# Kernel optimization log

Hardware: AMD Instinct MI355X
Metric: run time of the kernel (lower is better)

Reference implementation:

```python
import jax, jax.numpy as jnp
import numpy as np

D = 64   # hidden dim (input_dim == hidden_dims[i] == 64)
L = 6    # GNN layers per NBFNet
EPS = 1e-5

def _layer_norm(x, g, b):
    m = jnp.mean(x, axis=-1, keepdims=True)
    v = jnp.var(x, axis=-1, keepdims=True)
    return (x - m) * jax.lax.rsqrt(v + EPS) * g + b

def _conv(x, boundary, relation, edge_index, edge_type, W, b, g, bt):
    # GeneralizedRelationalConv: distmult message, sum aggregation with
    # boundary self-loop message, linear([input, agg]) -> LayerNorm -> ReLU.
    src, dst = edge_index[0], edge_index[1]
    msg = x[:, src, :] * relation[:, edge_type, :]                # [B,E,D]
    agg = boundary + jnp.zeros_like(x).at[:, dst, :].add(msg)     # edge_weight == 1
    out = jnp.einsum('bnf,fo->bno', jnp.concatenate([x, agg], axis=-1), W) + b
    return jax.nn.relu(_layer_norm(out, g, bt))

def _rel_model(q_rel, rel_edge_index, rel_edge_type, num_rel_nodes,
               rel_emb, Wr, br, gr, btr):
    # RelNBFNet.bellmanford: query = ones, boundary scatter at query relation node.
    B = q_rel.shape[0]
    query = jnp.ones((B, D), dtype=rel_emb.dtype)
    boundary = jnp.zeros((B, num_rel_nodes, D), rel_emb.dtype).at[jnp.arange(B), q_rel].add(query)
    relation = jnp.broadcast_to(rel_emb[None], (B,) + rel_emb.shape)  # dependent=False embedding
    def step(x, p):
        W, b, g, bt = p
        h = _conv(x, boundary, relation, rel_edge_index, rel_edge_type, W, b, g, bt)
        return h + x, None  # short_cut residual
    x, _ = jax.lax.scan(step, boundary, (Wr, br, gr, btr))
    return x  # [B, R, D]  (concat_hidden=False -> hiddens[-1])

def _ent_model(rel_repr, h_index, r_index, t_index, edge_index, edge_type,
               num_nodes, Wp1, bp1, Wp2, bp2, We, be, ge, bte, W1, b1, W2, b2):
    B = h_index.shape[0]
    query = rel_repr[jnp.arange(B), r_index]                      # [B,D]
    boundary = jnp.zeros((B, num_nodes, D), query.dtype).at[jnp.arange(B), h_index].add(query)
    def step(x, p):
        wp1, b1p, wp2, b2p, W, b, g, bt = p
        # project_relations=True: per-layer 2-layer MLP on relation representations
        rel = jax.nn.relu(rel_repr @ wp1 + b1p) @ wp2 + b2p       # [B,R,D]
        h = _conv(x, boundary, rel, edge_index, edge_type, W, b, g, bt)
        return h + x, None
    x, _ = jax.lax.scan(step, boundary, (Wp1, bp1, Wp2, bp2, We, be, ge, bte))
    node_query = jnp.broadcast_to(query[:, None, :], x.shape)
    feat = jnp.concatenate([x, node_query], axis=-1)              # [B,N,2D]
    feat = feat[jnp.arange(B)[:, None], t_index]                  # gather tails [B,K,2D]
    h = jax.nn.relu(feat @ W1 + b1)                               # num_mlp_layers=2
    return (h @ W2 + b2)[..., 0]                                  # [B,K]

def setup_inputs() -> dict:
    key = jax.random.key(0)
    ks = jax.random.split(key, 16)
    B, K, N, E, R, Er = 4, 256, 20000, 200000, 200, 4000
    ND = 100  # direct relations; R = 2*ND
    h = jax.random.randint(ks[0], (B,), 0, N)
    r = jax.random.randint(ks[1], (B,), 0, ND)
    t = jax.random.randint(ks[2], (B, K), 0, N)
    batch = jnp.stack([jnp.broadcast_to(h[:, None], (B, K)), t,
                       jnp.broadcast_to(r[:, None], (B, K))], axis=-1)
    s = 0.05
    return dict(
        batch=batch,
        edge_index=jax.random.randint(ks[3], (2, E), 0, N),
        edge_type=jax.random.randint(ks[4], (E,), 0, R),
        rel_edge_index=jax.random.randint(ks[5], (2, Er), 0, R),
        rel_edge_type=jax.random.randint(ks[6], (Er,), 0, 4),
        num_nodes=N, num_rel_nodes=R,
        rel_emb=jax.random.normal(ks[7], (4, D)) * s,
        Wr=jax.random.normal(ks[8], (L, 2 * D, D)) * s,
        br=jnp.zeros((L, D)), gr=jnp.ones((L, D)), btr=jnp.zeros((L, D)),
        Wp1=jax.random.normal(ks[9], (L, D, D)) * s,
        bp1=jnp.zeros((L, D)),
        Wp2=jax.random.normal(ks[10], (L, D, D)) * s,
        bp2=jnp.zeros((L, D)),
        We=jax.random.normal(ks[11], (L, 2 * D, D)) * s,
        be=jnp.zeros((L, D)), ge=jnp.ones((L, D)), bte=jnp.zeros((L, D)),
        W1=jax.random.normal(ks[12], (2 * D, 2 * D)) * s,
        b1=jnp.zeros((2 * D,)),
        W2=jax.random.normal(ks[13], (2 * D, 1)) * s,
        b2=jnp.zeros((1,)),
    )

def reference(batch, edge_index, edge_type, rel_edge_index, rel_edge_type,
              num_nodes, num_rel_nodes,
              rel_emb, Wr, br, gr, btr,
              Wp1, bp1, Wp2, bp2, We, be, ge, bte, W1, b1, W2, b2):
    # batch holds tail-negative triples (h, t, r) with constant h and r per row,
    # so negative_sample_to_tail is the identity here (eval mode: no edge removal).
    h_index = batch[:, 0, 0]
    t_index = batch[:, :, 1]
    r_index = batch[:, 0, 2]
    rel_repr = _rel_model(r_index, rel_edge_index, rel_edge_type, num_rel_nodes,
                          rel_emb, Wr, br, gr, btr)
    return _ent_model(rel_repr, h_index, r_index, t_index, edge_index, edge_type,
                      num_nodes, Wp1, bp1, Wp2, bp2, We, be, ge, bte, W1, b1, W2, b2)
```

## Files before the change

kernel.cpp:

```cpp
#include <hip/hip_runtime.h>
#include <hip/hip_bf16.h>

#define D_   64
#define L_   6
#define B_   4
#define K_   256
#define NN   20000
#define EE   200000
#define RR   200
#define ER_  4000
#define EPS_ 1e-5f

typedef unsigned short u16;
typedef unsigned int   u32;
typedef short bf16x8 __attribute__((ext_vector_type(8)));
typedef float f32x4  __attribute__((ext_vector_type(4)));

__device__ __forceinline__ u16 f2bf(float f) {
    u32 u = __float_as_uint(f);
    u += 0x7FFF + ((u >> 16) & 1);
    return (u16)(u >> 16);
}
__device__ __forceinline__ u32 pack2bf(float a, float b) {
    return (u32)f2bf(a) | ((u32)f2bf(b) << 16);
}
__device__ __forceinline__ float bflo(u32 u) { return __uint_as_float(u << 16); }
__device__ __forceinline__ float bfhi(u32 u) { return __uint_as_float(u & 0xFFFF0000u); }

__global__ __launch_bounds__(256)
void k_zero2(int* __restrict__ ec, int* __restrict__ rc) {
    int i = blockIdx.x * 256 + threadIdx.x;
    if (i < NN) ec[i] = 0;
    else if (i < NN + RR) rc[i - NN] = 0;
}

__global__ __launch_bounds__(256)
void k_hist2(const int* __restrict__ ei, const int* __restrict__ rei,
             int* __restrict__ ec, int* __restrict__ rc) {
    int g = blockIdx.x * 256 + threadIdx.x;
    if (g < EE) atomicAdd(&ec[ei[EE + g]], 1);
    else if (g < EE + ER_) atomicAdd(&rc[rei[ER_ + (g - EE)]], 1);
}

__global__ __launch_bounds__(256)
void k_scan1_2(const int* __restrict__ e_counts, int* __restrict__ e_pre, int* __restrict__ e_bs,
               const int* __restrict__ r_counts, int* __restrict__ r_pre, int* __restrict__ r_bs,
               int ent_nb) {
    __shared__ int tsum[256];
    const int* counts; int* pre; int* bs; int n; int blk;
    if ((int)blockIdx.x < ent_nb) { counts = e_counts; pre = e_pre; bs = e_bs; n = NN; blk = blockIdx.x; }
    else                          { counts = r_counts; pre = r_pre; bs = r_bs; n = RR; blk = 0; }
    int tid = threadIdx.x;
    int base = blk * 1024 + tid * 4;
    int c0 = 0, c1 = 0, c2 = 0, c3 = 0;
    if (base + 0 < n) c0 = counts[base + 0];
    if (base + 1 < n) c1 = counts[base + 1];
    if (base + 2 < n) c2 = counts[base + 2];
    if (base + 3 < n) c3 = counts[base + 3];
    tsum[tid] = c0 + c1 + c2 + c3;
    __syncthreads();
    if (tid == 0) {
        int acc = 0;
        for (int i = 0; i < 256; i++) { int t = tsum[i]; tsum[i] = acc; acc += t; }
    }
    __syncthreads();
    int run = tsum[tid];
    if (base + 0 < n) pre[base + 0] = run; run += c0;
    if (base + 1 < n) pre[base + 1] = run; run += c1;
    if (base + 2 < n) pre[base + 2] = run; run += c2;
    if (base + 3 < n) pre[base + 3] = run; run += c3;
    if (tid == 255) bs[blk] = run;
}

__global__ __launch_bounds__(64)
void k_scan2_2(int* __restrict__ eb, int enb, int* __restrict__ etot,
               int* __restrict__ rb, int rnb, int* __restrict__ rtot) {
    if (threadIdx.x == 0) {
        int acc = 0;
        for (int i = 0; i < enb; i++) { int t = eb[i]; eb[i] = acc; acc += t; }
        *etot = acc;
    }
    if (threadIdx.x == 1) {
        int acc = 0;
        for (int i = 0; i < rnb; i++) { int t = rb[i]; rb[i] = acc; acc += t; }
        *rtot = acc;
    }
}

__global__ __launch_bounds__(256)
void k_scan3_2(int* __restrict__ e_rp, const int* __restrict__ e_bs, int* __restrict__ e_cur,
               int* __restrict__ r_rp, const int* __restrict__ r_bs, int* __restrict__ r_cur) {
    int i = blockIdx.x * 256 + threadIdx.x;
    if (i < NN) {
        int v = e_rp[i] + e_bs[i >> 10];
        e_rp[i] = v; e_cur[i] = v;
    } else if (i < NN + RR) {
        int j = i - NN;
        int v = r_rp[j] + r_bs[j >> 10];
        r_rp[j] = v; r_cur[j] = v;
    }
}

__global__ __launch_bounds__(256)
void k_fill2(const int* __restrict__ ei, const int* __restrict__ et,
             const int* __restrict__ rei, const int* __restrict__ ret,
             int* __restrict__ e_cur, int* __restrict__ r_cur,
             int* __restrict__ e_packed, int* __restrict__ r_packed) {
    int g = blockIdx.x * 256 + threadIdx.x;
    if (g < EE) {
        int pos = atomicAdd(&e_cur[ei[EE + g]], 1);
        e_packed[pos] = ei[g] | (et[g] << 15);
    } else if (g < EE + ER_) {
        int h = g - EE;
        int pos = atomicAdd(&r_cur[rei[ER_ + h]], 1);
        r_packed[pos] = rei[h] | (ret[h] << 15);
    }
}

template<int NNODES, int MODE, bool FIRST>
__global__ __launch_bounds__(256)
void k_layer9(const float* __restrict__ xin, float* __restrict__ xout,
              const u16* __restrict__ xbin, u16* __restrict__ xbout,
              const void* __restrict__ relv,
              const int* __restrict__ rowptr, const int* __restrict__ packed,
              const float* __restrict__ query, const int* __restrict__ batch,
              const float* __restrict__ W, const float* __restrict__ bias,
              const float* __restrict__ gw, const float* __restrict__ bt) {
    __shared__ u16 Wt[64][72];
    __shared__ u16 As[16][72];
    __shared__ u16 Xs[16][72];
    __shared__ float LNbuf[16][68];
    const int tid   = threadIdx.x;
    const int node0 = blockIdx.x * 4;
    const int lane  = tid & 63;
    const int wv    = tid >> 6;

    int bn0 = batch[0 * K_ * 3 + (MODE ? 0 : 2)];
    int bn1 = batch[1 * K_ * 3 + (MODE ? 0 : 2)];
    int bn2 = batch[2 * K_ * 3 + (MODE ? 0 : 2)];
    int bn3 = batch[3 * K_ * 3 + (MODE ? 0 : 2)];

    const int gnode = node0 + wv;
    int beg = 0, end = 0;
    if (gnode < NNODES) { beg = rowptr[gnode]; end = rowptr[gnode + 1]; }

    const int erow  = wv * 4 + (lane >> 4);
    const int tx    = lane & 15;
    float4 resf = make_float4(0.f, 0.f, 0.f, 0.f);
    if constexpr (!FIRST) {
        int b = erow >> 2, nd = node0 + (erow & 3);
        if (nd < NNODES)
            resf = *reinterpret_cast<const float4*>(
                xin + ((size_t)b * NNODES + nd) * 64 + tx * 4);
    }

    {
        int n = lane, k16 = wv * 16;
        u32 buf[8];
        #pragma unroll
        for (int j2 = 0; j2 < 8; j2++) {
            float w0 = W[(64 + k16 + 2 * j2    ) * 64 + n];
            float w1 = W[(64 + k16 + 2 * j2 + 1) * 64 + n];
            buf[j2] = pack2bf(w0, w1);
        }
        uint4* dst = reinterpret_cast<uint4*>(&Wt[n][k16]);
        dst[0] = make_uint4(buf[0], buf[1], buf[2], buf[3]);
        dst[1] = make_uint4(buf[4], buf[5], buf[6], buf[7]);
    }

    if (tid < 128) {
        int m = tid >> 3, o8 = (tid & 7) * 8;
        int b = m >> 2, node = node0 + (m & 3);
        uint4 v = make_uint4(0, 0, 0, 0);
        if (node < NNODES) {
            if constexpr (FIRST) {
                int bnb = (b==0)?bn0:(b==1)?bn1:(b==2)?bn2:bn3;
                if (node == bnb) {
                    if constexpr (MODE == 1) {
                        const float* q = query + b * 64 + o8;
                        v = make_uint4(pack2bf(q[0], q[1]), pack2bf(q[2], q[3]),
                                       pack2bf(q[4], q[5]), pack2bf(q[6], q[7]));
                    } else {
                        v = make_uint4(0x3F803F80u, 0x3F803F80u, 0x3F803F80u, 0x3F803F80u);
                    }
                }
            } else if constexpr (MODE == 1) {
                v = *reinterpret_cast<const uint4*>(
                    xbin + ((size_t)b * NNODES + node) * 64 + o8);
            } else {
                const float* src = xin + ((size_t)b * NNODES + node) * 64 + o8;
                float4 x0 = *reinterpret_cast<const float4*>(src);
                float4 x1 = *reinterpret_cast<const float4*>(src + 4);
                v = make_uint4(pack2bf(x0.x, x0.y), pack2bf(x0.z, x0.w),
                               pack2bf(x1.x, x1.y), pack2bf(x1.z, x1.w));
            }
        }
        *reinterpret_cast<uint4*>(&Xs[m][o8]) = v;
    }

    const int slot = lane >> 3;
    const int d8   = lane & 7;

    float qreg[4][8];
    if constexpr (MODE == 1) {
        #pragma unroll
        for (int b = 0; b < 4; b++) {
            float4 q0 = *reinterpret_cast<const float4*>(query + b * 64 + d8 * 8);
            float4 q1 = *reinterpret_cast<const float4*>(query + b * 64 + d8 * 8 + 4);
            qreg[b][0]=q0.x; qreg[b][1]=q0.y; qreg[b][2]=q0.z; qreg[b][3]=q0.w;
            qreg[b][4]=q1.x; qreg[b][5]=q1.y; qreg[b][6]=q1.z; qreg[b][7]=q1.w;
        }
    }

    {
        float acc[4][8];
        #pragma unroll
        for (int b = 0; b < 4; b++)
            #pragma unroll
            for (int i = 0; i < 8; i++) acc[b][i] = 0.f;

        for (int e0 = beg; e0 < end; e0 += 16) {
            #pragma unroll
            for (int half = 0; half < 2; half++) {
                int e = e0 + half * 8 + slot;
                if (e < end) {
                    int p = packed[e];
                    int src = p & 0x7FFF;
                    int et  = p >> 15;
                    if constexpr (MODE == 1) {
                        const u16* rb = (const u16*)relv;
                        if constexpr (FIRST) {
                            #pragma unroll
                            for (int b = 0; b < 4; b++) {
                                int bnb = (b==0)?bn0:(b==1)?bn1:(b==2)?bn2:bn3;
                                if (src == bnb) {
                                    uint4 rv = *reinterpret_cast<const uint4*>(
                                        rb + ((size_t)(b * RR + et)) * 64 + d8 * 8);
                                    acc[b][0] = fmaf(qreg[b][0], bflo(rv.x), acc[b][0]);
                                    acc[b][1] = fmaf(qreg[b][1], bfhi(rv.x), acc[b][1]);
                                    acc[b][2] = fmaf(qreg[b][2], bflo(rv.y), acc[b][2]);
                                    acc[b][3] = fmaf(qreg[b][3], bfhi(rv.y), acc[b][3]);
                                    acc[b][4] = fmaf(qreg[b][4], bflo(rv.z), acc[b][4]);
                                    acc[b][5] = fmaf(qreg[b][5], bfhi(rv.z), acc[b][5]);
                                    acc[b][6] = fmaf(qreg[b][6], bflo(rv.w), acc[b][6]);
                                    acc[b][7] = fmaf(qreg[b][7], bfhi(rv.w), acc[b][7]);
                                }
                            }
                        } else {
                            #pragma unroll
                            for (int b = 0; b < 4; b++) {
                                uint4 xv = *reinterpret_cast<const uint4*>(
                                    xbin + ((size_t)(b * NNODES + src)) * 64 + d8 * 8);
                                uint4 rv = *reinterpret_cast<const uint4*>(
                                    ((const u16*)relv) + ((size_t)(b * RR + et)) * 64 + d8 * 8);
                                acc[b][0] = fmaf(bflo(xv.x), bflo(rv.x), acc[b][0]);
                                acc[b][1] = fmaf(bfhi(xv.x), bfhi(rv.x), acc[b][1]);
                                acc[b][2] = fmaf(bflo(xv.y), bflo(rv.y), acc[b][2]);
                                acc[b][3] = fmaf(bfhi(xv.y), bfhi(rv.y), acc[b][3]);
                                acc[b][4] = fmaf(bflo(xv.z), bflo(rv.z), acc[b][4]);
                                acc[b][5] = fmaf(bfhi(xv.z), bfhi(rv.z), acc[b][5]);
                                acc[b][6] = fmaf(bflo(xv.w), bflo(rv.w), acc[b][6]);
                                acc[b][7] = fmaf(bfhi(xv.w), bfhi(rv.w), acc[b][7]);
                            }
                        }
                    } else {
                        const float* re = (const float*)relv;
                        if constexpr (FIRST) {
                            bool m0 = (src == bn0), m1 = (src == bn1),
                                 m2 = (src == bn2), m3 = (src == bn3);
                            if (m0 | m1 | m2 | m3) {
                                float4 r0 = *reinterpret_cast<const float4*>(re + et * 64 + d8 * 8);
                                float4 r1 = *reinterpret_cast<const float4*>(re + et * 64 + d8 * 8 + 4);
                                float rr[8] = {r0.x,r0.y,r0.z,r0.w,r1.x,r1.y,r1.z,r1.w};
                                if (m0) {
                                    #pragma unroll
                                    for (int i = 0; i < 8; i++) acc[0][i] += rr[i];
                                }
                                if (m1) {
                                    #pragma unroll
                                    for (int i = 0; i < 8; i++) acc[1][i] += rr[i];
                                }
                                if (m2) {
                                    #pragma unroll
                                    for (int i = 0; i < 8; i++) acc[2][i] += rr[i];
                                }
                                if (m3) {
                                    #pragma unroll
                                    for (int i = 0; i < 8; i++) acc[3][i] += rr[i];
                                }
                            }
                        } else {
                            float4 r0 = *reinterpret_cast<const float4*>(re + et * 64 + d8 * 8);
                            float4 r1 = *reinterpret_cast<const float4*>(re + et * 64 + d8 * 8 + 4);
                            #pragma unroll
                            for (int b = 0; b < 4; b++) {
                                const float* xr = xin + ((size_t)(b * NNODES + src)) * 64 + d8 * 8;
                                float4 x0 = *reinterpret_cast<const float4*>(xr);
                                float4 x1 = *reinterpret_cast<const float4*>(xr + 4);
                                acc[b][0] = fmaf(x0.x, r0.x, acc[b][0]);
                                acc[b][1] = fmaf(x0.y, r0.y, acc[b][1]);
                                acc[b][2] = fmaf(x0.z, r0.z, acc[b][2]);
                                acc[b][3] = fmaf(x0.w, r0.w, acc[b][3]);
                                acc[b][4] = fmaf(x1.x, r1.x, acc[b][4]);
                                acc[b][5] = fmaf(x1.y, r1.y, acc[b][5]);
                                acc[b][6] = fmaf(x1.z, r1.z, acc[b][6]);
                                acc[b][7] = fmaf(x1.w, r1.w, acc[b][7]);
                            }
                        }
                    }
                }
            }
        }

        #pragma unroll
        for (int b = 0; b < 4; b++)
            #pragma unroll
            for (int i = 0; i < 8; i++) {
                float v = acc[b][i];
                v += __shfl_xor(v, 8);
                v += __shfl_xor(v, 16);
                v += __shfl_xor(v, 32);
                acc[b][i] = v;
            }

        if (slot < 4) {
            float out[8];
            #pragma unroll
            for (int i = 0; i < 8; i++)
                out[i] = (slot==0) ? acc[0][i] : (slot==1) ? acc[1][i]
                       : (slot==2) ? acc[2][i] : acc[3][i];
            int bnb = (slot==0)?bn0:(slot==1)?bn1:(slot==2)?bn2:bn3;
            if (gnode < NNODES && gnode == bnb) {
                if constexpr (MODE == 1) {
                    #pragma unroll
                    for (int i = 0; i < 8; i++)
                        out[i] += (slot==0)?qreg[0][i]:(slot==1)?qreg[1][i]
                                 :(slot==2)?qreg[2][i]:qreg[3][i];
                } else {
                    #pragma unroll
                    for (int i = 0; i < 8; i++) out[i] += 1.0f;
                }
            }
            int m = slot * 4 + wv;
            *reinterpret_cast<uint4*>(&As[m][d8 * 8]) =
                make_uint4(pack2bf(out[0], out[1]), pack2bf(out[2], out[3]),
                           pack2bf(out[4], out[5]), pack2bf(out[6], out[7]));
        }
    }
    __syncthreads();

    const int al = lane & 15;
    const int ag = lane >> 4;
    const int nt = wv;
    f32x4 acc4 = (f32x4){0.f, 0.f, 0.f, 0.f};
    {
        bf16x8 a0 = *reinterpret_cast<const bf16x8*>(&As[al][ag * 8]);
        bf16x8 a1 = *reinterpret_cast<const bf16x8*>(&As[al][32 + ag * 8]);
        bf16x8 b0 = *reinterpret_cast<const bf16x8*>(&Wt[nt * 16 + al][ag * 8]);
        bf16x8 b1 = *reinterpret_cast<const bf16x8*>(&Wt[nt * 16 + al][32 + ag * 8]);
        acc4 = __builtin_amdgcn_mfma_f32_16x16x32_bf16(a0, b0, acc4, 0, 0, 0);
        acc4 = __builtin_amdgcn_mfma_f32_16x16x32_bf16(a1, b1, acc4, 0, 0, 0);
    }
    __syncthreads();

    {
        int n = lane, k16 = wv * 16;
        u32 buf[8];
        #pragma unroll
        for (int j2 = 0; j2 < 8; j2++) {
            float w0 = W[(k16 + 2 * j2    ) * 64 + n];
            float w1 = W[(k16 + 2 * j2 + 1) * 64 + n];
            buf[j2] = pack2bf(w0, w1);
        }
        uint4* dst = reinterpret_cast<uint4*>(&Wt[n][k16]);
        dst[0] = make_uint4(buf[0], buf[1], buf[2], buf[3]);
        dst[1] = make_uint4(buf[4], buf[5], buf[6], buf[7]);
    }
    __syncthreads();

    {
        bf16x8 x0 = *reinterpret_cast<const bf16x8*>(&Xs[al][ag * 8]);
        bf16x8 x1 = *reinterpret_cast<const bf16x8*>(&Xs[al][32 + ag * 8]);
        bf16x8 b0 = *reinterpret_cast<const bf16x8*>(&Wt[nt * 16 + al][ag * 8]);
        bf16x8 b1 = *reinterpret_cast<const bf16x8*>(&Wt[nt * 16 + al][32 + ag * 8]);
        acc4 = __builtin_amdgcn_mfma_f32_16x16x32_bf16(x0, b0, acc4, 0, 0, 0);
        acc4 = __builtin_amdgcn_mfma_f32_16x16x32_bf16(x1, b1, acc4, 0, 0, 0);
    }
    #pragma unroll
    for (int reg = 0; reg < 4; reg++)
        LNbuf[ag * 4 + reg][nt * 16 + al] = acc4[reg];
    __syncthreads();

    {
        int row = erow;
        int b = row >> 2, node = node0 + (row & 3);
        float o[4];
        float s1 = 0.f, s2 = 0.f;
        #pragma unroll
        for (int i = 0; i < 4; i++) {
            o[i] = LNbuf[row][tx * 4 + i] + bias[tx * 4 + i];
            s1 += o[i];
            s2 += o[i] * o[i];
        }
        s1 += __shfl_xor(s1, 1); s2 += __shfl_xor(s2, 1);
        s1 += __shfl_xor(s1, 2); s2 += __shfl_xor(s2, 2);
        s1 += __shfl_xor(s1, 4); s2 += __shfl_xor(s2, 4);
        s1 += __shfl_xor(s1, 8); s2 += __shfl_xor(s2, 8);
        float mean = s1 * (1.f / 64.f);
        float var  = s2 * (1.f / 64.f) - mean * mean;
        float inv  = rsqrtf(var + EPS_);
        if (node < NNODES) {
            int bnb = (b==0)?bn0:(b==1)?bn1:(b==2)?bn2:bn3;
            size_t ro = ((size_t)b * NNODES + node) * 64;
            float r[4] = {resf.x, resf.y, resf.z, resf.w};
            if constexpr (FIRST) {
                r[0] = r[1] = r[2] = r[3] = 0.f;
                if (node == bnb) {
                    if constexpr (MODE == 1) {
                        float4 q = *reinterpret_cast<const float4*>(query + b * 64 + tx * 4);
                        r[0] = q.x; r[1] = q.y; r[2] = q.z; r[3] = q.w;
                    } else {
                        r[0] = r[1] = r[2] = r[3] = 1.0f;
                    }
                }
            }
            float nv[4];
            #pragma unroll
            for (int i = 0; i < 4; i++) {
                float h = (o[i] - mean) * inv * gw[tx * 4 + i] + bt[tx * 4 + i];
                h = fmaxf(h, 0.f);
                nv[i] = r[i] + h;
            }
            *reinterpret_cast<float4*>(&xout[ro + tx * 4]) =
                make_float4(nv[0], nv[1], nv[2], nv[3]);
            if constexpr (MODE == 1) {
                ushort4 b4;
                b4.x = f2bf(nv[0]); b4.y = f2bf(nv[1]);
                b4.z = f2bf(nv[2]); b4.w = f2bf(nv[3]);
                *reinterpret_cast<ushort4*>(&xbout[ro + tx * 4]) = b4;
            }
        }
    }
}

__global__ __launch_bounds__(64)
void k_rel_mlp_all(const float* __restrict__ rel_repr,
                   const float* __restrict__ Wp1, const float* __restrict__ bp1,
                   const float* __restrict__ Wp2, const float* __restrict__ bp2,
                   u16* __restrict__ out) {
    __shared__ float rowv[64];
    __shared__ float hid[64];
    int l     = blockIdx.x / (B_ * RR);
    int rowid = blockIdx.x % (B_ * RR);
    int d = threadIdx.x;
    const float* w1 = Wp1 + l * 4096;
    const float* w2 = Wp2 + l * 4096;
    rowv[d] = rel_repr[rowid * 64 + d];
    __syncthreads();
    float acc = bp1[l * 64 + d];
    for (int k = 0; k < 64; k++) acc = fmaf(rowv[k], w1[k * 64 + d], acc);
    hid[d] = fmaxf(acc, 0.f);
    __syncthreads();
    float o = bp2[l * 64 + d];
    for (int k = 0; k < 64; k++) o = fmaf(hid[k], w2[k * 64 + d], o);
    out[(size_t)l * B_ * RR * 64 + rowid * 64 + d] = f2bf(o);
}

__global__ __launch_bounds__(256)
void k_query(const float* __restrict__ rel_repr, const int* __restrict__ batch,
             float* __restrict__ query) {
    int tid = threadIdx.x;
    int b = tid >> 6;
    int d = tid & 63;
    int r = batch[b * K_ * 3 + 2];
    query[b * 64 + d] = rel_repr[(b * RR + r) * 64 + d];
}

__global__ __launch_bounds__(128)
void k_final(const float* __restrict__ x, const float* __restrict__ query,
             const int* __restrict__ batch,
             const float* __restrict__ W1, const float* __restrict__ b1,
             const float* __restrict__ W2, const float* __restrict__ b2,
             float* __restrict__ out) {
    __shared__ float feat[128];
    __shared__ float partial[2];
    int pair = blockIdx.x;
    int b = pair / K_;
    int t = batch[pair * 3 + 1];
    int d = threadIdx.x;
    feat[d] = (d < 64) ? x[(size_t)(b * NN + t) * 64 + d] : query[b * 64 + (d - 64)];
    __syncthreads();
    float h = b1[d];
    for (int i = 0; i < 128; i++) h = fmaf(feat[i], W1[i * 128 + d], h);
    h = fmaxf(h, 0.f);
    float v = h * W2[d];
    #pragma unroll
    for (int off = 1; off < 64; off <<= 1) v += __shfl_xor(v, off);
    if ((d & 63) == 0) partial[d >> 6] = v;
    __syncthreads();
    if (d == 0) out[pair] = partial[0] + partial[1] + b2[0];
}

extern "C" void kernel_launch(void* const* d_in, const int* in_sizes, int n_in,
                              void* d_out, int out_size, void* d_ws, size_t ws_size,
                              hipStream_t stream) {
    const int* batch      = (const int*)d_in[0];
    const int* edge_index = (const int*)d_in[1];
    const int* edge_type  = (const int*)d_in[2];
    const int* rel_ei     = (const int*)d_in[3];
    const int* rel_et     = (const int*)d_in[4];
    const float* rel_emb = (const float*)d_in[7];
    const float* Wr  = (const float*)d_in[8];
    const float* br  = (const float*)d_in[9];
    const float* gr  = (const float*)d_in[10];
    const float* btr = (const float*)d_in[11];
    const float* Wp1 = (const float*)d_in[12];
    const float* bp1 = (const float*)d_in[13];
    const float* Wp2 = (const float*)d_in[14];
    const float* bp2 = (const float*)d_in[15];
    const float* We  = (const float*)d_in[16];
    const float* be  = (const float*)d_in[17];
    const float* ge  = (const float*)d_in[18];
    const float* bte = (const float*)d_in[19];
    const float* W1  = (const float*)d_in[20];
    const float* b1  = (const float*)d_in[21];
    const float* W2  = (const float*)d_in[22];
    const float* b2  = (const float*)d_in[23];

    float* ws = (float*)d_ws;
    float* rel_buf0 = ws;
    float* rel_buf1 = rel_buf0 + 51200;
    float* query    = rel_buf1 + 51200;
    float* x0       = query + 256;
    float* x1       = x0 + (size_t)B_ * NN * 64;
    u16*   xb0      = (u16*)(x1 + (size_t)B_ * NN * 64);
    u16*   xb1      = xb0 + (size_t)B_ * NN * 64;
    u16*   rel_all  = xb1 + (size_t)B_ * NN * 64;
    int*   iw       = (int*)(rel_all + (size_t)L_ * B_ * RR * 64);

    int* ent_counts  = iw;
    int* ent_rowptr  = ent_counts + NN;
    int* ent_bsums   = ent_rowptr + NN + 1;
    int* ent_packed  = ent_bsums + 32;
    int* rel_counts  = ent_packed + EE;
    int* rel_rowptr  = rel_counts + RR;
    int* rel_bsums   = rel_rowptr + RR + 1;
    int* rel_packed  = rel_bsums + 8;

    const int ENT_NB = (NN + 1023) / 1024;
    const int REL_NB = (RR + 1023) / 1024;

    k_zero2<<<(NN + RR + 255) / 256, 256, 0, stream>>>(ent_counts, rel_counts);
    k_hist2<<<(EE + ER_ + 255) / 256, 256, 0, stream>>>(edge_index, rel_ei, ent_counts, rel_counts);
    k_scan1_2<<<ENT_NB + REL_NB, 256, 0, stream>>>(ent_counts, ent_rowptr, ent_bsums,
                                                   rel_counts, rel_rowptr, rel_bsums, ENT_NB);
    k_scan2_2<<<1, 64, 0, stream>>>(ent_bsums, ENT_NB, ent_rowptr + NN,
                                    rel_bsums, REL_NB, rel_rowptr + RR);
    k_scan3_2<<<(NN + RR + 255) / 256, 256, 0, stream>>>(ent_rowptr, ent_bsums, ent_counts,
                                                         rel_rowptr, rel_bsums, rel_counts);
    k_fill2<<<(EE + ER_ + 255) / 256, 256, 0, stream>>>(edge_index, edge_type, rel_ei, rel_et,
                                                        ent_counts, rel_counts, ent_packed, rel_packed);

    float* rf[2] = {rel_buf0, rel_buf1};
    const int RGRID = (RR + 3) / 4;
    k_layer9<RR, 0, true><<<RGRID, 256, 0, stream>>>(
        nullptr, rf[0], nullptr, nullptr, rel_emb,
        rel_rowptr, rel_packed, nullptr, batch,
        Wr, br, gr, btr);
    int rc = 0;
    for (int l = 1; l < L_; ++l) {
        k_layer9<RR, 0, false><<<RGRID, 256, 0, stream>>>(
            rf[rc], rf[rc ^ 1], nullptr, nullptr, rel_emb,
            rel_rowptr, rel_packed, nullptr, batch,
            Wr + l * 8192, br + l * 64, gr + l * 64, btr + l * 64);
        rc ^= 1;
    }
    float* rel_final = rf[rc];

    k_query<<<1, 256, 0, stream>>>(rel_final, batch, query);
    k_rel_mlp_all<<<L_ * B_ * RR, 64, 0, stream>>>(rel_final, Wp1, bp1, Wp2, bp2, rel_all);
    float* xf[2] = {x0, x1};
    u16*   xh[2] = {xb0, xb1};
    const int EGRID = (NN + 3) / 4;
    k_layer9<NN, 1, true><<<EGRID, 256, 0, stream>>>(
        nullptr, xf[0], nullptr, xh[0], rel_all,
        ent_rowptr, ent_packed, query, batch,
        We, be, ge, bte);
    int ec = 0;
    for (int l = 1; l < L_; ++l) {
        k_layer9<NN, 1, false><<<EGRID, 256, 0, stream>>>(
            xf[ec], xf[ec ^ 1], xh[ec], xh[ec ^ 1],
            rel_all + (size_t)l * B_ * RR * 64,
            ent_rowptr, ent_packed, query, batch,
            We + l * 8192, be + l * 64, ge + l * 64, bte + l * 64);
        ec ^= 1;
    }
    k_final<<<B_ * K_, 128, 0, stream>>>(xf[ec], query, batch, W1, b1, W2, b2,
                                         (float*)d_out);
}
```

Before: 400.7 us.

## Sort nodes by in-degree so each block processes nodes with similar edge counts

Adds three preprocessing kernels that bucket nodes by in-degree (capped at 63), prefix-sum the buckets and build a permutation array. Each layer kernel then maps block slots to nodes through this permutation, so the four waves in a block gather similar numbers of edges. This targets load imbalance, where a block waits on its highest-degree node. The cost is extra launches, an indirect lookup per node, and scattered, less-coalesced reads and writes of node rows.

```diff
diff --git a/kernel.cpp b/kernel.cpp
--- a/kernel.cpp
+++ b/kernel.cpp
@@ -28,10 +28,13 @@
 __device__ __forceinline__ float bfhi(u32 u) { return __uint_as_float(u & 0xFFFF0000u); }
 
 __global__ __launch_bounds__(256)
-void k_zero2(int* __restrict__ ec, int* __restrict__ rc) {
+void k_zero2(int* __restrict__ ec, int* __restrict__ rc,
+             int* __restrict__ ebc, int* __restrict__ rbc) {
     int i = blockIdx.x * 256 + threadIdx.x;
     if (i < NN) ec[i] = 0;
     else if (i < NN + RR) rc[i - NN] = 0;
+    else if (i < NN + RR + 64) ebc[i - NN - RR] = 0;
+    else if (i < NN + RR + 128) rbc[i - NN - RR - 64] = 0;
 }
 
 __global__ __launch_bounds__(256)
@@ -117,12 +120,57 @@
     }
 }
 
+__global__ __launch_bounds__(256)
+void k_degcount(const int* __restrict__ e_rp, const int* __restrict__ r_rp,
+                int* __restrict__ e_bc, int* __restrict__ r_bc) {
+    int i = blockIdx.x * 256 + threadIdx.x;
+    if (i < NN) {
+        int d = e_rp[i + 1] - e_rp[i]; if (d > 63) d = 63;
+        atomicAdd(&e_bc[d], 1);
+    } else if (i < NN + RR) {
+        int j = i - NN;
+        int d = r_rp[j + 1] - r_rp[j]; if (d > 63) d = 63;
+        atomicAdd(&r_bc[d], 1);
+    }
+}
+
+__global__ __launch_bounds__(64)
+void k_degscan(int* __restrict__ e_bc, int* __restrict__ e_bcur,
+               int* __restrict__ r_bc, int* __restrict__ r_bcur) {
+    if (threadIdx.x == 0) {
+        int a = 0;
+        for (int i = 0; i < 64; i++) { int t = e_bc[i]; e_bc[i] = a; e_bcur[i] = a; a += t; }
+    }
+    if (threadIdx.x == 1) {
+        int a = 0;
+        for (int i = 0; i < 64; i++) { int t = r_bc[i]; r_bc[i] = a; r_bcur[i] = a; a += t; }
+    }
+}
+
+__global__ __launch_bounds__(256)
+void k_degscatter(const int* __restrict__ e_rp, const int* __restrict__ r_rp,
+                  int* __restrict__ e_bcur, int* __restrict__ r_bcur,
+                  int* __restrict__ e_perm, int* __restrict__ r_perm) {
+    int i = blockIdx.x * 256 + threadIdx.x;
+    if (i < NN) {
+        int d = e_rp[i + 1] - e_rp[i]; if (d > 63) d = 63;
+        int pos = atomicAdd(&e_bcur[d], 1);
+        e_perm[pos] = i;
+    } else if (i < NN + RR) {
+        int j = i - NN;
+        int d = r_rp[j + 1] - r_rp[j]; if (d > 63) d = 63;
+        int pos = atomicAdd(&r_bcur[d], 1);
+        r_perm[pos] = j;
+    }
+}
+
 template<int NNODES, int MODE, bool FIRST>
 __global__ __launch_bounds__(256)
 void k_layer9(const float* __restrict__ xin, float* __restrict__ xout,
               const u16* __restrict__ xbin, u16* __restrict__ xbout,
               const void* __restrict__ relv,
               const int* __restrict__ rowptr, const int* __restrict__ packed,
+              const int* __restrict__ perm,
               const float* __restrict__ query, const int* __restrict__ batch,
               const float* __restrict__ W, const float* __restrict__ bias,
               const float* __restrict__ gw, const float* __restrict__ bt) {
@@ -140,18 +188,23 @@
     int bn2 = batch[2 * K_ * 3 + (MODE ? 0 : 2)];
     int bn3 = batch[3 * K_ * 3 + (MODE ? 0 : 2)];
 
-    const int gnode = node0 + wv;
-    int beg = 0, end = 0;
-    if (gnode < NNODES) { beg = rowptr[gnode]; end = rowptr[gnode + 1]; }
+    const int gslot = node0 + wv;
+    int gnode = 0, beg = 0, end = 0;
+    if (gslot < NNODES) {
+        gnode = perm[gslot];
+        beg = rowptr[gnode]; end = rowptr[gnode + 1];
+    }
 
     const int erow  = wv * 4 + (lane >> 4);
     const int tx    = lane & 15;
     float4 resf = make_float4(0.f, 0.f, 0.f, 0.f);
     if constexpr (!FIRST) {
-        int b = erow >> 2, nd = node0 + (erow & 3);
-        if (nd < NNODES)
+        int b = erow >> 2, ns = node0 + (erow & 3);
+        if (ns < NNODES) {
+            int nd = perm[ns];
             resf = *reinterpret_cast<const float4*>(
                 xin + ((size_t)b * NNODES + nd) * 64 + tx * 4);
+        }
     }
 
     {
@@ -170,9 +223,10 @@
 
     if (tid < 128) {
         int m = tid >> 3, o8 = (tid & 7) * 8;
-        int b = m >> 2, node = node0 + (m & 3);
+        int b = m >> 2, ns = node0 + (m & 3);
         uint4 v = make_uint4(0, 0, 0, 0);
-        if (node < NNODES) {
+        if (ns < NNODES) {
+            int node = perm[ns];
             if constexpr (FIRST) {
                 int bnb = (b==0)?bn0:(b==1)?bn1:(b==2)?bn2:bn3;
                 if (node == bnb) {
@@ -330,7 +384,7 @@
                 out[i] = (slot==0) ? acc[0][i] : (slot==1) ? acc[1][i]
                        : (slot==2) ? acc[2][i] : acc[3][i];
             int bnb = (slot==0)?bn0:(slot==1)?bn1:(slot==2)?bn2:bn3;
-            if (gnode < NNODES && gnode == bnb) {
+            if (gslot < NNODES && gnode == bnb) {
                 if constexpr (MODE == 1) {
                     #pragma unroll
                     for (int i = 0; i < 8; i++)
@@ -393,7 +447,7 @@
 
     {
         int row = erow;
-        int b = row >> 2, node = node0 + (row & 3);
+        int b = row >> 2, ns = node0 + (row & 3);
         float o[4];
         float s1 = 0.f, s2 = 0.f;
         #pragma unroll
@@ -409,7 +463,8 @@
         float mean = s1 * (1.f / 64.f);
         float var  = s2 * (1.f / 64.f) - mean * mean;
         float inv  = rsqrtf(var + EPS_);
-        if (node < NNODES) {
+        if (ns < NNODES) {
+            int node = perm[ns];
             int bnb = (b==0)?bn0:(b==1)?bn1:(b==2)?bn2:bn3;
             size_t ro = ((size_t)b * NNODES + node) * 64;
             float r[4] = {resf.x, resf.y, resf.z, resf.w};
@@ -546,11 +601,17 @@
     int* rel_rowptr  = rel_counts + RR;
     int* rel_bsums   = rel_rowptr + RR + 1;
     int* rel_packed  = rel_bsums + 8;
+    int* e_bc        = rel_packed + ER_;
+    int* r_bc        = e_bc + 64;
+    int* e_bcur      = r_bc + 64;
+    int* r_bcur      = e_bcur + 64;
+    int* e_perm      = r_bcur + 64;
+    int* r_perm      = e_perm + NN;
 
     const int ENT_NB = (NN + 1023) / 1024;
     const int REL_NB = (RR + 1023) / 1024;
 
-    k_zero2<<<(NN + RR + 255) / 256, 256, 0, stream>>>(ent_counts, rel_counts);
+    k_zero2<<<(NN + RR + 128 + 255) / 256, 256, 0, stream>>>(ent_counts, rel_counts, e_bc, r_bc);
     k_hist2<<<(EE + ER_ + 255) / 256, 256, 0, stream>>>(edge_index, rel_ei, ent_counts, rel_counts);
     k_scan1_2<<<ENT_NB + REL_NB, 256, 0, stream>>>(ent_counts, ent_rowptr, ent_bsums,
                                                    rel_counts, rel_rowptr, rel_bsums, ENT_NB);
@@ -560,18 +621,22 @@
                                                          rel_rowptr, rel_bsums, rel_counts);
     k_fill2<<<(EE + ER_ + 255) / 256, 256, 0, stream>>>(edge_index, edge_type, rel_ei, rel_et,
                                                         ent_counts, rel_counts, ent_packed, rel_packed);
+    k_degcount<<<(NN + RR + 255) / 256, 256, 0, stream>>>(ent_rowptr, rel_rowptr, e_bc, r_bc);
+    k_degscan<<<1, 64, 0, stream>>>(e_bc, e_bcur, r_bc, r_bcur);
+    k_degscatter<<<(NN + RR + 255) / 256, 256, 0, stream>>>(ent_rowptr, rel_rowptr,
+                                                            e_bcur, r_bcur, e_perm, r_perm);
 
     float* rf[2] = {rel_buf0, rel_buf1};
     const int RGRID = (RR + 3) / 4;
     k_layer9<RR, 0, true><<<RGRID, 256, 0, stream>>>(
         nullptr, rf[0], nullptr, nullptr, rel_emb,
-        rel_rowptr, rel_packed, nullptr, batch,
+        rel_rowptr, rel_packed, r_perm, nullptr, batch,
         Wr, br, gr, btr);
     int rc = 0;
     for (int l = 1; l < L_; ++l) {
         k_layer9<RR, 0, false><<<RGRID, 256, 0, stream>>>(
             rf[rc], rf[rc ^ 1], nullptr, nullptr, rel_emb,
-            rel_rowptr, rel_packed, nullptr, batch,
+            rel_rowptr, rel_packed, r_perm, nullptr, batch,
             Wr + l * 8192, br + l * 64, gr + l * 64, btr + l * 64);
         rc ^= 1;
     }
@@ -584,14 +649,14 @@
     const int EGRID = (NN + 3) / 4;
     k_layer9<NN, 1, true><<<EGRID, 256, 0, stream>>>(
         nullptr, xf[0], nullptr, xh[0], rel_all,
-        ent_rowptr, ent_packed, query, batch,
+        ent_rowptr, ent_packed, e_perm, query, batch,
         We, be, ge, bte);
     int ec = 0;
     for (int l = 1; l < L_; ++l) {
         k_layer9<NN, 1, false><<<EGRID, 256, 0, stream>>>(
             xf[ec], xf[ec ^ 1], xh[ec], xh[ec ^ 1],
             rel_all + (size_t)l * B_ * RR * 64,
-            ent_rowptr, ent_packed, query, batch,
+            ent_rowptr, ent_packed, e_perm, query, batch,
             We + l * 8192, be + l * 64, ge + l * 64, bte + l * 64);
         ec ^= 1;
     }
```

Result: slower. 556.5 us (+38.9%).
